# Kernel optimization log

Measured on AMD Instinct MI355X. Metric: run time of the kernel, lower is better.

## Reference

```python
import jax, jax.numpy as jnp
import numpy as np
from jax import lax

NUM_CLASSES = 80
STRIDES = (8, 16, 32, 64, 128)
PRE_NMS_THRESH = 0.05
PRE_NMS_TOPK = 1000
NMS_THRESH = 0.6
POST_NMS_TOPK = 100
NUM_CONVS = 4
CIN = 256
BATCH = 2
FEAT_SHAPES = ((100, 152), (50, 76), (25, 38), (13, 19), (7, 10))
CLASS_OFFSET = 10000.0  # coordinate offset for class-aware NMS


def conv3x3(x, w, b):
    # x: [B,C,H,W], w: [O,C,3,3] -> [B,O,H,W], stride 1, SAME padding
    y = lax.conv_general_dilated(x, w, (1, 1), 'SAME',
                                 dimension_numbers=('NCHW', 'OIHW', 'NCHW'))
    return y + b[None, :, None, None]


def tower(x, Ws, Bs):
    # sequence of (conv3x3 -> ReLU), norm='none'
    for i in range(Ws.shape[0]):
        x = jax.nn.relu(conv3x3(x, Ws[i], Bs[i]))
    return x


def compute_locations(h, w, stride):
    sx = jnp.arange(w, dtype=jnp.float32) * stride
    sy = jnp.arange(h, dtype=jnp.float32) * stride
    yy, xx = jnp.meshgrid(sy, sx, indexing='ij')
    return jnp.stack([xx.reshape(-1), yy.reshape(-1)], axis=1) + stride // 2  # [HW,2]


def nms_single(boxes, scores, classes):
    # boxes [N,4], scores [N] (>=0), classes [N] int. Greedy class-aware NMS.
    off = classes.astype(boxes.dtype) * CLASS_OFFSET
    b = boxes + off[:, None]
    area = (b[:, 2] - b[:, 0]) * (b[:, 3] - b[:, 1])

    def step(s, _):
        i = jnp.argmax(s)
        v = s[i]
        bi = b[i]
        lt = jnp.maximum(bi[:2], b[:, :2])
        rb = jnp.minimum(bi[2:], b[:, 2:])
        wh = jnp.maximum(rb - lt, 0.0)
        inter = wh[:, 0] * wh[:, 1]
        iou = inter / (area[i] + area - inter + 1e-9)
        s2 = jnp.where(iou > NMS_THRESH, -1.0, s).at[i].set(-1.0)
        return s2, (i, v)

    _, (idx, vals) = lax.scan(step, scores, None, length=POST_NMS_TOPK)
    valid = vals > 0.0
    out = jnp.concatenate(
        [boxes[idx], vals[:, None], classes[idx].astype(boxes.dtype)[:, None]], axis=1)
    return jnp.where(valid[:, None], out, 0.0)  # [POST_NMS_TOPK, 6]


def _forward(p3, p4, p5, p6, p7, cls_w, cls_b, box_w, box_b,
             logit_w, logit_b, pred_w, pred_b, ctr_w, ctr_b, scales):
    feats = (p3, p4, p5, p6, p7)
    boxes_all, scores_all, cls_all = [], [], []
    for l, x in enumerate(feats):
        # share_tower has 0 convs -> identity
        ct = tower(x, cls_w, cls_b)
        bt = tower(x, box_w, box_b)
        logits = conv3x3(ct, logit_w, logit_b)                   # [B,C,H,W]
        ctr = conv3x3(bt, ctr_w, ctr_b)                          # [B,1,H,W]
        reg = jax.nn.relu(conv3x3(bt, pred_w, pred_b) * scales[l])  # [B,4,H,W]
        B, _, H, W = logits.shape
        HW = H * W
        locs = compute_locations(H, W, STRIDES[l])               # [HW,2]
        cls_prob = jax.nn.sigmoid(logits).transpose(0, 2, 3, 1).reshape(B, HW, NUM_CLASSES)
        ctr_prob = jax.nn.sigmoid(ctr).reshape(B, HW, 1)
        s = cls_prob * ctr_prob                                  # thresh_with_ctr
        s = jnp.where(s > PRE_NMS_THRESH, s, 0.0)
        k = min(PRE_NMS_TOPK, HW * NUM_CLASSES)
        vals, idx = lax.top_k(s.reshape(B, HW * NUM_CLASSES), k)
        loc_idx = idx // NUM_CLASSES                             # [B,k]
        cls_idx = idx % NUM_CLASSES
        reg_f = reg.transpose(0, 2, 3, 1).reshape(B, HW, 4)
        reg_sel = jnp.take_along_axis(reg_f, loc_idx[..., None], axis=1)  # [B,k,4]
        loc_sel = locs[loc_idx]                                  # [B,k,2]
        boxes = jnp.stack([loc_sel[..., 0] - reg_sel[..., 0],
                           loc_sel[..., 1] - reg_sel[..., 1],
                           loc_sel[..., 0] + reg_sel[..., 2],
                           loc_sel[..., 1] + reg_sel[..., 3]], axis=-1)
        boxes_all.append(boxes)
        scores_all.append(jnp.sqrt(jnp.maximum(vals, 1e-12)))
        cls_all.append(cls_idx)
    boxes = jnp.concatenate(boxes_all, axis=1)    # [B,N,4]
    scores = jnp.concatenate(scores_all, axis=1)  # [B,N]
    classes = jnp.concatenate(cls_all, axis=1)    # [B,N]
    return jax.vmap(nms_single)(boxes, scores, classes)  # [B,POST_NMS_TOPK,6]


def setup_inputs() -> dict:
    key = jax.random.key(0)
    ks = jax.random.split(key, 12)
    std = 0.05  # larger than fcos init std=0.01 so decoded scores exceed the threshold
    inp = {}
    for i, (h, w) in enumerate(FEAT_SHAPES):
        inp[f'p{i + 3}'] = jax.random.normal(ks[i], (BATCH, CIN, h, w), dtype=jnp.float32)
    inp['cls_w'] = jax.random.normal(ks[5], (NUM_CONVS, CIN, CIN, 3, 3), dtype=jnp.float32) * std
    inp['cls_b'] = jnp.zeros((NUM_CONVS, CIN), dtype=jnp.float32)
    inp['box_w'] = jax.random.normal(ks[6], (NUM_CONVS, CIN, CIN, 3, 3), dtype=jnp.float32) * std
    inp['box_b'] = jnp.zeros((NUM_CONVS, CIN), dtype=jnp.float32)
    inp['logit_w'] = jax.random.normal(ks[7], (NUM_CLASSES, CIN, 3, 3), dtype=jnp.float32) * std
    inp['logit_b'] = jnp.zeros((NUM_CLASSES,), dtype=jnp.float32)
    inp['pred_w'] = jax.random.normal(ks[8], (4, CIN, 3, 3), dtype=jnp.float32) * std
    inp['pred_b'] = jnp.zeros((4,), dtype=jnp.float32)
    inp['ctr_w'] = jax.random.normal(ks[9], (1, CIN, 3, 3), dtype=jnp.float32) * std
    inp['ctr_b'] = jnp.zeros((1,), dtype=jnp.float32)
    inp['scales'] = jnp.ones((5,), dtype=jnp.float32)
    return inp


def reference(p3, p4, p5, p6, p7, cls_w, cls_b, box_w, box_b,
              logit_w, logit_b, pred_w, pred_b, ctr_w, ctr_b, scales):
    return _forward(p3, p4, p5, p6, p7, cls_w, cls_b, box_w, box_b,
                    logit_w, logit_b, pred_w, pred_b, ctr_w, ctr_b, scales)
```

## Files before the change

### kernel.cpp

```cpp
#include <hip/hip_runtime.h>
#include <stdint.h>
#include <math.h>

#define NCLS 80
#define TOTHW 20267
#define WLAYER 1179648ull

typedef _Float16 f16x8 __attribute__((ext_vector_type(8)));
typedef float f32x4 __attribute__((ext_vector_type(4)));
typedef short s16x8 __attribute__((ext_vector_type(8)));

static constexpr int cLW[5]    = {152,76,38,19,10};
static constexpr int cLH[5]    = {100,50,25,13,7};
static constexpr int cLHW[5]   = {15200,3800,950,247,70};
static constexpr int cLCUM[5]  = {0,15200,19000,19950,20197};
static constexpr int cLSTR[5]  = {8,16,32,64,128};
static constexpr int cCB[11]   = {0,123,246,278,310,319,328,331,334,335,336};
static constexpr int cPBASE[11]= {0,15744,31488,35584,39680,40832,41984,42368,42752,42880,43008};
static constexpr int cRCUM[11] = {0,100,200,250,300,325,350,363,376,383,390};
static constexpr int cCPX64[6] = {0,475,594,624,632,635};
#define NPXB64 635
#define SBE 11010048ull

__device__ __forceinline__ void split2(float y, unsigned short& h0, unsigned short& h1) {
  _Float16 b0 = (_Float16)y;
  float f0 = (float)b0;
  _Float16 b1 = (_Float16)((y - f0) * 2048.0f);
  h0 = __builtin_bit_cast(unsigned short, b0);
  h1 = __builtin_bit_cast(unsigned short, b1);
}

__device__ __forceinline__ void lds_hist_add(uint32_t* h, uint32_t bucket) {
  unsigned long long act = __ballot(1);
  int lane = (int)(threadIdx.x & 63u);
  int leader = __ffsll(act) - 1;
  uint32_t lb = (uint32_t)__shfl((int)bucket, leader, 64);
  unsigned long long same = __ballot(bucket == lb);
  if (same == act) {
    if (lane == leader) atomicAdd(&h[bucket], (uint32_t)__popcll(act));
  } else {
    atomicAdd(&h[bucket], 1u);
  }
}

__global__ void k_zero(unsigned short* X0, unsigned short* X1) {
  int px = blockIdx.x * 256 + threadIdx.x;
  if (px >= 43008) return;
  int pi = 0;
#pragma unroll
  for (int i = 1; i < 10; i++) if (px >= cPBASE[i]) pi = i;
  const int l = pi >> 1;
  const int p = px - cPBASE[pi];
  const int W = cLW[l], H = cLH[l], PWl = W + 2;
  const int pr = p / PWl, pc = p - pr * PWl;
  if (pr >= 1 && pr <= H && pc >= 1 && pc <= W) return;
  s16x8 z = {0,0,0,0,0,0,0,0};
  size_t base = (size_t)px * 256;
#pragma unroll
  for (int k = 0; k < 32; k++) {
    *reinterpret_cast<s16x8*>(X0 + base + k*8) = z;
    *reinterpret_cast<s16x8*>(X1 + base + k*8) = z;
  }
}

__global__ __launch_bounds__(256)
void k_prep(const float* __restrict__ p0, const float* __restrict__ p1,
            const float* __restrict__ p2, const float* __restrict__ p3,
            const float* __restrict__ p4,
            unsigned short* __restrict__ X0, unsigned short* __restrict__ X1) {
  int bx = blockIdx.x;
  int pi = 0;
#pragma unroll
  for (int i = 1; i < 10; i++) if (bx >= cRCUM[i]) pi = i;
  const int h = bx - cRCUM[pi];
  const int l = pi >> 1, bidx = pi & 1;
  const int W = cLW[l], HW = cLHW[l], PWl = W + 2;
  const int PB = cPBASE[pi];
  const float* src;
  if (l == 0) src = p0; else if (l == 1) src = p1; else if (l == 2) src = p2;
  else if (l == 3) src = p3; else src = p4;
  src += (size_t)bidx * 256 * HW;
  const int tid = threadIdx.x;
  __shared__ float tile[64][152];
  for (int c0 = 0; c0 < 256; c0 += 64) {
    {
      int c = tid >> 2, wq = tid & 3;
      for (int w = wq; w < W; w += 4)
        tile[c][w] = src[(size_t)(c0 + c) * HW + h * W + w];
    }
    __syncthreads();
    {
      int c8 = (tid & 7) * 8;
      for (int w = tid >> 3; w < W; w += 32) {
        size_t base = (size_t)(PB + (h + 1) * PWl + (w + 1)) * 256 + c0 + c8;
        unsigned short a0[8], a1[8];
#pragma unroll
        for (int j = 0; j < 8; j++) split2(tile[c8 + j][w], a0[j], a1[j]);
        *reinterpret_cast<s16x8*>(X0 + base) = *reinterpret_cast<s16x8*>(a0);
        *reinterpret_cast<s16x8*>(X1 + base) = *reinterpret_cast<s16x8*>(a1);
      }
    }
    __syncthreads();
  }
}

__global__ void k_packall(const float* __restrict__ box_w, const float* __restrict__ cls_w,
                          const float* __restrict__ logit_w, unsigned short* __restrict__ wp) {
  const int layer = blockIdx.y;
  const int oc = blockIdx.x, c = threadIdx.x;
  const float* w; int Cout = 256;
  const size_t WSTRIDE = (size_t)256 * 2304;
  if (layer < 4)      w = box_w + (size_t)layer * WSTRIDE;
  else if (layer < 8) w = cls_w + (size_t)(layer - 4) * WSTRIDE;
  else { w = logit_w; Cout = NCLS; }
  if (oc >= Cout) return;
  unsigned short* wpL = wp + (size_t)layer * WLAYER;
  const int ocf = oc >> 4, ln = oc & 15;
  const int kc = c >> 5, kg = (c >> 3) & 3, e = c & 7;
  const int lane = kg * 16 + ln;
#pragma unroll
  for (int r = 0; r < 9; r++) {
    float v = w[((size_t)oc * 256 + c) * 9 + r];
    unsigned short h0, h1;
    split2(v, h0, h1);
    wpL[((((size_t)(r * 2 + 0) * 16 + ocf) * 8 + kc) * 64 + lane) * 8 + e] = h0;
    wpL[((((size_t)(r * 2 + 1) * 16 + ocf) * 8 + kc) * 64 + lane) * 8 + e] = h1;
  }
}

__global__ void k_packhead(const float* __restrict__ ctw, const float* __restrict__ pdw,
                           float* __restrict__ wh) {
  const int r = blockIdx.x, c = threadIdx.x;
  float* d = &wh[((size_t)r * 256 + c) * 5];
  d[0] = ctw[c * 9 + r];
#pragma unroll
  for (int q = 0; q < 4; q++) d[1 + q] = pdw[(size_t)q * 2304 + c * 9 + r];
}

struct MfArgs {
  const unsigned short *X0, *X1;
  const unsigned short *Wp;
  const float* bias;
  unsigned short *Y0, *Y1;
  float* actf;
  float* scores;
  const float* ctrp;
  uint32_t* hist;
};

template<int EPI>
__global__ __launch_bounds__(256, 2)
void conv_mfma(MfArgs a) {
  __shared__ __align__(16) unsigned short lds[18432];
  const int tid = threadIdx.x;
  const int lane = tid & 63;
  const int wid = tid >> 6;

  const int nwg = (EPI == 2) ? 336 : 672;
  const int id = blockIdx.x;
  const int w = (id & 7) * (nwg >> 3) + (id >> 3);
  const int oc0 = (EPI == 2) ? 0 : (w & 1) * 128;
  int bx = (EPI == 2) ? w : (w >> 1);

  int pi = 0;
#pragma unroll
  for (int i = 1; i < 10; i++) if (bx >= cCB[i]) pi = i;
  const int l = pi >> 1, bidx = pi & 1;
  const int pxb = bx - cCB[pi];
  const int px0 = pxb * 128;
  const int PB = cPBASE[pi];
  const int W = cLW[l], H = cLH[l], HW = cLHW[l], PWl = W + 2;

  int row_[2], g_[2];
#pragma unroll
  for (int d = 0; d < 2; d++) {
    int idx2 = tid + d * 256;
    row_[d] = idx2 >> 2;
    g_[d] = idx2 & 3;
  }

  const int wr = wid >> 1, wc = wid & 1;
  const int kg = lane >> 4, ln15 = lane & 15;
  int fA[4];
#pragma unroll
  for (int mt = 0; mt < 4; mt++) fA[mt] = (wr * 64 + mt * 16 + ln15) * 72 + kg * 8;
  const int ocfb = (oc0 >> 4) + wc * 4;

  f32x4 acc0[4][4], acc1[4][4];
#pragma unroll
  for (int mt = 0; mt < 4; mt++)
#pragma unroll
    for (int nt = 0; nt < 4; nt++) {
      acc0[mt][nt] = (f32x4){0.f, 0.f, 0.f, 0.f};
      acc1[mt][nt] = (f32x4){0.f, 0.f, 0.f, 0.f};
    }

  s16x8 ra[4];
  auto loadA = [&](int step) {
    const int rr = step >> 3;
    const int c0 = (step & 7) << 5;
    const int dh = rr / 3 - 1, dw = rr - (rr / 3) * 3 - 1;
    const long long OFF = (long long)(PB + px0 + dh * PWl + dw);
#pragma unroll
    for (int s = 0; s < 2; s++) {
      const unsigned short* Xs = (s == 0) ? a.X0 : a.X1;
#pragma unroll
      for (int d = 0; d < 2; d++)
        ra[s * 2 + d] = *reinterpret_cast<const s16x8*>(Xs + (OFF + row_[d]) * 256 + c0 + g_[d] * 8);
    }
  };
  auto writeA = [&](int buf) {
#pragma unroll
    for (int s = 0; s < 2; s++)
#pragma unroll
      for (int d = 0; d < 2; d++) {
        const int o = buf * 9216 + row_[d] * 72 + (s * 4 + g_[d]) * 8;
        *reinterpret_cast<s16x8*>(&lds[o]) = ra[s * 2 + d];
      }
  };
  auto loadB = [&](int step, f16x8* bv) {
    const int rr = step >> 3, cc = step & 7;
#pragma unroll
    for (int nt = 0; nt < 4; nt++) {
      const size_t bo = ((size_t)((rr * 2) * 16 + ocfb + nt) * 8 + cc) * 512 + lane * 8;
      bv[nt * 2 + 0] = *reinterpret_cast<const f16x8*>(a.Wp + bo);
      bv[nt * 2 + 1] = *reinterpret_cast<const f16x8*>(a.Wp + bo + 65536);
    }
  };
  auto mfmaStep = [&](int buf, const f16x8* bv) {
    f16x8 av[4][2];
#pragma unroll
    for (int mt = 0; mt < 4; mt++) {
      av[mt][0] = *reinterpret_cast<const f16x8*>(&lds[buf * 9216 + fA[mt]]);
      av[mt][1] = *reinterpret_cast<const f16x8*>(&lds[buf * 9216 + fA[mt] + 32]);
    }
#pragma unroll
    for (int mt = 0; mt < 4; mt++)
#pragma unroll
      for (int nt = 0; nt < 4; nt++) {
        acc0[mt][nt] = __builtin_amdgcn_mfma_f32_16x16x32_f16(av[mt][0], bv[nt * 2 + 0], acc0[mt][nt], 0, 0, 0);
        acc1[mt][nt] = __builtin_amdgcn_mfma_f32_16x16x32_f16(av[mt][0], bv[nt * 2 + 1], acc1[mt][nt], 0, 0, 0);
        acc1[mt][nt] = __builtin_amdgcn_mfma_f32_16x16x32_f16(av[mt][1], bv[nt * 2 + 0], acc1[mt][nt], 0, 0, 0);
      }
  };

  f16x8 bv0[8], bv1[8];
  loadA(0); writeA(0);
  loadA(1);
  loadB(0, bv0);
  __syncthreads();

  for (int sp = 0; sp < 72; sp += 2) {
    if (sp + 1 < 72) { writeA(1); loadB(sp + 1, bv1); }
    if (sp + 2 < 72) loadA(sp + 2);
    mfmaStep(0, bv0);
    __syncthreads();
    if (sp + 2 < 72) { writeA(0); loadB(sp + 2, bv0); }
    if (sp + 3 < 72) loadA(sp + 3);
    mfmaStep(1, bv1);
    __syncthreads();
  }

  uint32_t* hh = nullptr;
  if (EPI == 2) {
    hh = reinterpret_cast<uint32_t*>(lds);
    for (int i = tid; i < 4096; i += 256) hh[i] = 0;
    __syncthreads();
  }
#pragma unroll
  for (int mt = 0; mt < 4; mt++) {
#pragma unroll
    for (int i = 0; i < 4; i++) {
      const int pxl = wr * 64 + mt * 16 + (lane >> 4) * 4 + i;
      const int p = px0 + pxl;
      const int pr = p / PWl, pc = p - pr * PWl;
      if (!(pr >= 1 && pr <= H && pc >= 1 && pc <= W)) continue;
      const int hw = (pr - 1) * W + (pc - 1);
#pragma unroll
      for (int nt = 0; nt < 4; nt++) {
        const int oc = oc0 + wc * 64 + nt * 16 + ln15;
        const float v = acc0[mt][nt][i] + acc1[mt][nt][i] * 4.8828125e-4f;
        if (EPI == 2) {
          if (oc < NCLS) {
            float y = v + a.bias[oc];
            float pcs = 1.0f / (1.0f + expf(-y));
            float s = pcs * a.ctrp[2 * cLCUM[l] + bidx * HW + hw];
            s = (s > 0.05f) ? s : 0.f;
            a.scores[(size_t)NCLS * (2 * cLCUM[l] + bidx * HW) + (size_t)oc * HW + hw] = s;
            lds_hist_add(hh, __float_as_uint(s) >> 20);
          }
        } else {
          float y = fmaxf(v + a.bias[oc], 0.f);
          if (EPI == 0) {
            size_t o = (size_t)(PB + p) * 256 + oc;
            unsigned short h0, h1;
            split2(y, h0, h1);
            a.Y0[o] = h0; a.Y1[o] = h1;
          } else {
            a.actf[(size_t)(PB + p) * 256 + oc] = y;
          }
        }
      }
    }
  }
  if (EPI == 2) {
    __syncthreads();
    uint32_t* gh = a.hist + (size_t)(l * 2 + bidx) * 4096;
    for (int i = tid; i < 4096; i += 256) { uint32_t v = hh[i]; if (v) atomicAdd(&gh[i], v); }
  }
}

__global__ __launch_bounds__(256)
void k_head2(const float* __restrict__ headact, const float* __restrict__ wh,
             const float* __restrict__ ctb, const float* __restrict__ pdb,
             const float* __restrict__ scl,
             float* __restrict__ ctrp, float* __restrict__ regb) {
  __shared__ float swh[11520];
  for (int i = threadIdx.x; i < 11520; i += 256) swh[i] = wh[i];
  int bx = blockIdx.x; int l = 0;
#pragma unroll
  for (int i = 1; i < 5; i++) if (bx >= cCPX64[i]) l = i;
  const int lblk = bx - cCPX64[l];
  const int H = cLH[l], W = cLW[l], HW = cLHW[l]; const int N = 2 * HW;
  const int lane = threadIdx.x & 63;
  const int wv = threadIdx.x >> 6;
  __syncthreads();
  const float bb0 = ctb[0], bb1 = pdb[0], bb2 = pdb[1], bb3 = pdb[2], bb4 = pdb[3];
  const float sc = scl[l];
  const int c4 = lane * 4;
  for (int t = 0; t < 16; ++t) {
    int px = lblk * 64 + wv * 16 + t;
    if (px >= N) break;
    int bb = px / HW; int hw = px - bb * HW; int hh = hw / W; int ww = hw - hh * W;
    const int PB = cPBASE[l * 2 + bb];
    float a0 = 0.f, a1 = 0.f, a2 = 0.f, a3 = 0.f, a4 = 0.f;
#pragma unroll
    for (int r = 0; r < 9; r++) {
      int dh = r / 3 - 1, dw = r % 3 - 1;
      int ih = hh + dh, iw = ww + dw;
      if (!(((unsigned)ih < (unsigned)H) && ((unsigned)iw < (unsigned)W))) continue;
      const float4 x = *reinterpret_cast<const float4*>(
          headact + (size_t)(PB + (ih + 1) * (W + 2) + (iw + 1)) * 256 + c4);
      const float* wr = &swh[(size_t)(r * 256 + c4) * 5];
      a0 = fmaf(x.x, wr[0],  a0); a1 = fmaf(x.x, wr[1],  a1); a2 = fmaf(x.x, wr[2],  a2);
      a3 = fmaf(x.x, wr[3],  a3); a4 = fmaf(x.x, wr[4],  a4);
      a0 = fmaf(x.y, wr[5],  a0); a1 = fmaf(x.y, wr[6],  a1); a2 = fmaf(x.y, wr[7],  a2);
      a3 = fmaf(x.y, wr[8],  a3); a4 = fmaf(x.y, wr[9],  a4);
      a0 = fmaf(x.z, wr[10], a0); a1 = fmaf(x.z, wr[11], a1); a2 = fmaf(x.z, wr[12], a2);
      a3 = fmaf(x.z, wr[13], a3); a4 = fmaf(x.z, wr[14], a4);
      a0 = fmaf(x.w, wr[15], a0); a1 = fmaf(x.w, wr[16], a1); a2 = fmaf(x.w, wr[17], a2);
      a3 = fmaf(x.w, wr[18], a3); a4 = fmaf(x.w, wr[19], a4);
    }
#pragma unroll
    for (int off = 32; off > 0; off >>= 1) {
      a0 += __shfl_xor(a0, off, 64); a1 += __shfl_xor(a1, off, 64); a2 += __shfl_xor(a2, off, 64);
      a3 += __shfl_xor(a3, off, 64); a4 += __shfl_xor(a4, off, 64);
    }
    if (lane == 0) {
      const int gi = 2 * cLCUM[l] + bb * HW + hw;
      ctrp[gi] = 1.0f / (1.0f + expf(-(a0 + bb0)));
      float* rg = regb + (size_t)gi * 4;
      rg[0] = fmaxf((a1 + bb1) * sc, 0.f);
      rg[1] = fmaxf((a2 + bb2) * sc, 0.f);
      rg[2] = fmaxf((a3 + bb3) * sc, 0.f);
      rg[3] = fmaxf((a4 + bb4) * sc, 0.f);
    }
  }
}

__global__ void k_init(uint32_t* __restrict__ hist, uint32_t* __restrict__ ctrA,
                       uint32_t* __restrict__ ctrB, uint32_t* __restrict__ survCnt) {
  int i = blockIdx.x * blockDim.x + threadIdx.x;
  if (i < 40960) hist[i] = 0;
  if (i < 10) { ctrA[i] = 0; ctrB[i] = 0; }
  if (i < 2) survCnt[i] = 0;
}

__global__ __launch_bounds__(256)
void k_select(const uint32_t* __restrict__ hist, int* __restrict__ meta) {
  const int sid = blockIdx.x;
  const uint32_t* gh = hist + (size_t)sid * 4096;
  __shared__ uint32_t ps[256];
  uint32_t sum = 0;
  for (int i = 0; i < 16; i++) sum += gh[threadIdx.x * 16 + i];
  ps[threadIdx.x] = sum;
  __syncthreads();
  if (threadIdx.x == 0) {
    uint32_t c = 0; int T = 0, m = 1000;
    for (int ch = 255; ch >= 0; --ch) {
      if (c + ps[ch] >= 1000u) {
        for (int t = ch * 16 + 15; t >= ch * 16; --t) {
          uint32_t hv = gh[t];
          if (c + hv >= 1000u) { T = t; m = (int)(1000u - c); break; }
          c += hv;
        }
        break;
      }
      c += ps[ch];
    }
    meta[sid * 4 + 0] = T;
    meta[sid * 4 + 1] = (int)c;
    meta[sid * 4 + 2] = m;
    meta[sid * 4 + 3] = (int)gh[T];
  }
}

__global__ __launch_bounds__(256)
void k_collect(const float* __restrict__ scores, const int* __restrict__ meta,
               unsigned long long* __restrict__ listA, unsigned long long* __restrict__ listB,
               uint32_t* __restrict__ ctrA, uint32_t* __restrict__ ctrB) {
  const int sid = blockIdx.y; const int l = sid >> 1, b = sid & 1;
  const int HW = cLHW[l]; const int size = NCLS * HW;
  const int base = blockIdx.x * 4096;
  if (base >= size) return;
  const size_t sbase = (size_t)NCLS * (2 * cLCUM[l] + b * HW);
  const float* sb = scores + sbase;
  unsigned long long* lB = listB + sbase;
  unsigned long long* lA = listA + (size_t)sid * 1024;
  const uint32_t T = (uint32_t)meta[sid * 4];
  const int lane = (int)(threadIdx.x & 63u);
  __shared__ uint32_t cA, cB, bA, bB;
  if (threadIdx.x == 0) { cA = 0; cB = 0; }
  __syncthreads();
  uint32_t wa = 0, wb = 0;
  for (int j = 0; j < 16; j++) {
    int i = base + threadIdx.x + j * 256;
    bool inb = (i < size);
    uint32_t bits = inb ? __float_as_uint(sb[i]) : 0u;
    uint32_t bkt = bits >> 20;
    unsigned long long mA = __ballot(inb && bkt > T);
    unsigned long long mB = __ballot(inb && bkt == T);
    if (lane == 0) { wa += (uint32_t)__popcll(mA); wb += (uint32_t)__popcll(mB); }
  }
  if (lane == 0) { if (wa) atomicAdd(&cA, wa); if (wb) atomicAdd(&cB, wb); }
  __syncthreads();
  if (threadIdx.x == 0) {
    bA = cA ? atomicAdd(&ctrA[sid], cA) : 0u;
    bB = cB ? atomicAdd(&ctrB[sid], cB) : 0u;
    cA = 0; cB = 0;
  }
  __syncthreads();
  for (int j = 0; j < 16; j++) {
    int i = base + threadIdx.x + j * 256;
    bool inb = (i < size);
    uint32_t bits = inb ? __float_as_uint(sb[i]) : 0u;
    uint32_t bkt = bits >> 20;
    bool pA = inb && bkt > T;
    bool pB = inb && bkt == T;
    unsigned long long key = 0;
    if (pA || pB) {
      int cls = i / HW; int hw = i - cls * HW;
      uint32_t idx = (uint32_t)(hw * NCLS + cls);
      key = ((unsigned long long)bits << 32) | (unsigned long long)(0xFFFFFFFFu - idx);
    }
    unsigned long long mA = __ballot(pA);
    unsigned long long mB = __ballot(pB);
    unsigned long long lt = (1ull << lane) - 1ull;
    if (mA) {
      int ld = __ffsll(mA) - 1;
      uint32_t wbs = 0;
      if (lane == ld) wbs = atomicAdd(&cA, (uint32_t)__popcll(mA));
      wbs = (uint32_t)__shfl((int)wbs, ld, 64);
      if (pA) {
        uint32_t pos = bA + wbs + (uint32_t)__popcll(mA & lt);
        if (pos < 1024u) lA[pos] = key;
      }
    }
    if (mB) {
      int ld = __ffsll(mB) - 1;
      uint32_t wbs = 0;
      if (lane == ld) wbs = atomicAdd(&cB, (uint32_t)__popcll(mB));
      wbs = (uint32_t)__shfl((int)wbs, ld, 64);
      if (pB) lB[bB + wbs + (uint32_t)__popcll(mB & lt)] = key;
    }
  }
}

__global__ __launch_bounds__(1024)
void k_refine(const int* __restrict__ meta, const unsigned long long* __restrict__ listB,
              unsigned long long* __restrict__ listA, uint32_t* __restrict__ ctrA) {
  const int sid = blockIdx.x; const int l = sid >> 1, b = sid & 1;
  const int HW = cLHW[l];
  const size_t sbase = (size_t)NCLS * (2 * cLCUM[l] + b * HW);
  const unsigned long long* lB = listB + sbase;
  const int nB = meta[sid * 4 + 3];
  int m = meta[sid * 4 + 2];
  __shared__ uint32_t h[256];
  __shared__ unsigned long long sPre;
  __shared__ int sM;
  __shared__ uint32_t sCnt;
  unsigned long long prefix = 0, mask = 0;
  for (int p = 7; p >= 0; --p) {
    for (int i = threadIdx.x; i < 256; i += 1024) h[i] = 0;
    __syncthreads();
    for (int i = threadIdx.x; i < nB; i += 1024) {
      unsigned long long k = lB[i];
      if ((k & mask) == prefix) {
        uint32_t bkt = (uint32_t)((k >> (p * 8)) & 255ull);
        lds_hist_add(h, bkt);
      }
    }
    __syncthreads();
    if (threadIdx.x == 0) {
      uint32_t c = 0; int sel = 0; int mnew = m;
      for (int t = 255; t >= 0; --t) {
        if (c + h[t] >= (uint32_t)m) { sel = t; mnew = m - (int)c; break; }
        c += h[t];
      }
      sPre = prefix | ((unsigned long long)sel << (p * 8));
      sM = mnew;
    }
    __syncthreads();
    prefix = sPre; m = sM;
    mask |= (0xFFull << (p * 8));
    __syncthreads();
  }
  if (threadIdx.x == 0) sCnt = ctrA[sid];
  __syncthreads();
  for (int i = threadIdx.x; i < nB; i += 1024) {
    unsigned long long k = lB[i];
    if (k >= prefix) {
      uint32_t pos = atomicAdd(&sCnt, 1u);
      if (pos < 1024u) listA[(size_t)sid * 1024 + pos] = k;
    }
  }
  __syncthreads();
  if (threadIdx.x == 0) ctrA[sid] = sCnt;
}

__global__ __launch_bounds__(256)
void k_sortdec(const unsigned long long* __restrict__ listA, const uint32_t* __restrict__ ctrA,
               const float* __restrict__ regb, float* __restrict__ cbox,
               float* __restrict__ cscr, float* __restrict__ ccls) {
  const int sid = blockIdx.x; const int l = sid >> 1, b = sid & 1;
  const int HW = cLHW[l], W = cLW[l];
  __shared__ unsigned long long key[1024];
  int n = (int)ctrA[sid]; if (n > 1024) n = 1024;
  for (int i = threadIdx.x; i < 1024; i += 256)
    key[i] = (i < n) ? listA[(size_t)sid * 1024 + i] : 0ull;
  __syncthreads();
  for (int len = 2; len <= 1024; len <<= 1) {
    for (int j = len >> 1; j > 0; j >>= 1) {
      for (int t = threadIdx.x; t < 512; t += 256) {
        int i = ((t & ~(j - 1)) << 1) | (t & (j - 1));
        int pp = i | j;
        unsigned long long a = key[i], bq = key[pp];
        bool desc = ((i & len) == 0);
        if ((a < bq) == desc) { key[i] = bq; key[pp] = a; }
      }
      __syncthreads();
    }
  }
  for (int r = threadIdx.x; r < 1000; r += 256) {
    unsigned long long k = key[r];
    uint32_t bits = (uint32_t)(k >> 32);
    uint32_t idx = 0xFFFFFFFFu - (uint32_t)(k & 0xFFFFFFFFull);
    float val = __uint_as_float(bits);
    float sc = sqrtf(fmaxf(val, 1e-12f));
    int cls = (int)(idx % NCLS); int loc = (int)(idx / NCLS);
    int hh = loc / W; int ww = loc - hh * W;
    float cx = (float)(ww * cLSTR[l] + (cLSTR[l] >> 1));
    float cy = (float)(hh * cLSTR[l] + (cLSTR[l] >> 1));
    const float* rg = regb + (size_t)(2 * cLCUM[l] + b * HW + loc) * 4;
    int slot = b * 5000 + l * 1000 + r;
    cbox[slot * 4 + 0] = cx - rg[0];
    cbox[slot * 4 + 1] = cy - rg[1];
    cbox[slot * 4 + 2] = cx + rg[2];
    cbox[slot * 4 + 3] = cy + rg[3];
    cscr[slot] = sc;
    ccls[slot] = (float)cls;
  }
}

#define NMSC 1536
__global__ __launch_bounds__(256)
void k_nmscls(const float* __restrict__ cbox, const float* __restrict__ cscr,
              const float* __restrict__ ccls,
              unsigned long long* __restrict__ surv, uint32_t* __restrict__ survCnt) {
  const int cls = blockIdx.x;
  const int b = blockIdx.y;
  __shared__ unsigned short mslot[5024];
  __shared__ float ms[5024];
  __shared__ float kx1[NMSC], ky1[NMSC], kx2[NMSC], ky2[NMSC], kar[NMSC];
  __shared__ uint32_t mcnt;
  __shared__ int sPick; __shared__ float sPickV;
  __shared__ float pb[5];
  __shared__ float wvv[4]; __shared__ int wvi[4];
  if (threadIdx.x == 0) mcnt = 0;
  __syncthreads();
  const float fc = (float)cls;
  for (int j = threadIdx.x; j < 5000; j += 256) {
    if (ccls[b * 5000 + j] == fc) {
      uint32_t p = atomicAdd(&mcnt, 1u);
      mslot[p] = (unsigned short)j;
      ms[p] = cscr[b * 5000 + j];
    }
  }
  __syncthreads();
  const int n = (int)mcnt;
  if (n == 0) return;
  const float off = fc * 10000.0f;
  const int nc = n < NMSC ? n : NMSC;
  for (int i = threadIdx.x; i < nc; i += 256) {
    const float4 bq = *reinterpret_cast<const float4*>(cbox + ((size_t)b * 5000 + mslot[i]) * 4);
    float x1 = bq.x + off, y1 = bq.y + off, x2 = bq.z + off, y2 = bq.w + off;
    kx1[i] = x1; ky1[i] = y1; kx2[i] = x2; ky2[i] = y2; kar[i] = (x2 - x1) * (y2 - y1);
  }
  __syncthreads();
  const int lane = threadIdx.x & 63, wv = threadIdx.x >> 6;
  for (int it = 0; it < 100; ++it) {
    float best = -1.f; int bi = 0x7FFF; int bidx = 0;
    for (int i = threadIdx.x; i < n; i += 256) {
      float v = ms[i];
      int sl = mslot[i];
      if (v > best || (v == best && sl < bi)) { best = v; bi = sl; bidx = i; }
    }
    for (int o = 32; o > 0; o >>= 1) {
      float ov = __shfl_down(best, o, 64);
      int oi = __shfl_down(bi, o, 64);
      int ox = __shfl_down(bidx, o, 64);
      if (ov > best || (ov == best && oi < bi)) { best = ov; bi = oi; bidx = ox; }
    }
    if (lane == 0) { wvv[wv] = best; wvi[wv] = (bidx << 13) | bi; }
    __syncthreads();
    if (threadIdx.x == 0) {
      float bb = wvv[0]; int pk = wvi[0];
      for (int q = 1; q < 4; q++) {
        float v = wvv[q]; int c = wvi[q];
        if (v > bb || (v == bb && (c & 8191) < (pk & 8191))) { bb = v; pk = c; }
      }
      sPickV = bb; sPick = pk;
      if (bb >= 0.f) {
        int slot = pk & 8191;
        uint32_t bits = __float_as_uint(bb);
        uint32_t gslot = (uint32_t)(b * 5000 + slot);
        unsigned long long key = ((unsigned long long)bits << 32) |
                                 (unsigned long long)(0xFFFFFFFFu - gslot);
        uint32_t pos = atomicAdd(&survCnt[b], 1u);
        surv[(size_t)b * 5000 + pos] = key;
        const float4 bx = *reinterpret_cast<const float4*>(cbox + (size_t)gslot * 4);
        pb[0] = bx.x + off; pb[1] = bx.y + off; pb[2] = bx.z + off; pb[3] = bx.w + off;
        pb[4] = (pb[2] - pb[0]) * (pb[3] - pb[1]);
      }
    }
    __syncthreads();
    if (sPickV < 0.f) break;
    const int pidx = sPick >> 13;
    const float bx1 = pb[0], by1 = pb[1], bx2 = pb[2], by2 = pb[3], ba = pb[4];
    for (int i = threadIdx.x; i < n; i += 256) {
      float v = ms[i];
      if (v < 0.f) continue;
      float x1, y1, x2, y2, ar;
      if (i < NMSC) {
        x1 = kx1[i]; y1 = ky1[i]; x2 = kx2[i]; y2 = ky2[i]; ar = kar[i];
      } else {
        const float4 bq = *reinterpret_cast<const float4*>(cbox + ((size_t)b * 5000 + mslot[i]) * 4);
        x1 = bq.x + off; y1 = bq.y + off; x2 = bq.z + off; y2 = bq.w + off;
        ar = (x2 - x1) * (y2 - y1);
      }
      float ix1 = fmaxf(bx1, x1), iy1 = fmaxf(by1, y1);
      float ix2 = fminf(bx2, x2), iy2 = fminf(by2, y2);
      float iw = fmaxf(ix2 - ix1, 0.f), ih = fmaxf(iy2 - iy1, 0.f);
      float inter = iw * ih;
      float iou = inter / ((ba + ar - inter) + 1e-9f);
      if (iou > 0.6f || i == pidx) ms[i] = -1.0f;
    }
    __syncthreads();
  }
}

__global__ __launch_bounds__(1024)
void k_nmsfinal(const unsigned long long* __restrict__ surv, const uint32_t* __restrict__ survCnt,
                const float* __restrict__ cbox, const float* __restrict__ ccls,
                float* __restrict__ out) {
  const int b = blockIdx.x;
  const int n = (int)survCnt[b];
  const unsigned long long* sv = surv + (size_t)b * 5000;
  const int m = n < 100 ? n : 100;
  __shared__ uint32_t h[256];
  __shared__ unsigned long long sPre; __shared__ int sM;
  __shared__ unsigned long long topk[128];
  __shared__ uint32_t tcnt;
  unsigned long long prefix = 0, mask = 0;
  int mm = m;
  if (m > 0) {
    for (int p = 7; p >= 0; --p) {
      for (int i = threadIdx.x; i < 256; i += 1024) h[i] = 0;
      __syncthreads();
      for (int i = threadIdx.x; i < n; i += 1024) {
        unsigned long long k = sv[i];
        if ((k & mask) == prefix) lds_hist_add(h, (uint32_t)((k >> (p * 8)) & 255ull));
      }
      __syncthreads();
      if (threadIdx.x == 0) {
        uint32_t c = 0; int sel = 0; int mnew = mm;
        for (int t = 255; t >= 0; --t) {
          if (c + h[t] >= (uint32_t)mm) { sel = t; mnew = mm - (int)c; break; }
          c += h[t];
        }
        sPre = prefix | ((unsigned long long)sel << (p * 8));
        sM = mnew;
      }
      __syncthreads();
      prefix = sPre; mm = sM;
      mask |= (0xFFull << (p * 8));
      __syncthreads();
    }
  }
  if (threadIdx.x == 0) tcnt = 0;
  for (int i = threadIdx.x; i < 128; i += 1024) topk[i] = 0;
  __syncthreads();
  if (m > 0) {
    for (int i = threadIdx.x; i < n; i += 1024) {
      unsigned long long k = sv[i];
      if (k >= prefix) {
        uint32_t p = atomicAdd(&tcnt, 1u);
        if (p < 128) topk[p] = k;
      }
    }
  }
  __syncthreads();
  for (int len = 2; len <= 128; len <<= 1) {
    for (int j = len >> 1; j > 0; j >>= 1) {
      for (int t = threadIdx.x; t < 64; t += 1024) {
        int i = ((t & ~(j - 1)) << 1) | (t & (j - 1));
        int pp = i | j;
        unsigned long long a = topk[i], bq = topk[pp];
        bool desc = ((i & len) == 0);
        if ((a < bq) == desc) { topk[i] = bq; topk[pp] = a; }
      }
      __syncthreads();
    }
  }
  if (threadIdx.x < 100) {
    int it = threadIdx.x;
    float* orow = out + ((size_t)b * 100 + it) * 6;
    if (it < m) {
      unsigned long long k = topk[it];
      uint32_t gslot = 0xFFFFFFFFu - (uint32_t)(k & 0xFFFFFFFFull);
      const float4 bx = *reinterpret_cast<const float4*>(cbox + (size_t)gslot * 4);
      orow[0] = bx.x; orow[1] = bx.y; orow[2] = bx.z; orow[3] = bx.w;
      orow[4] = __uint_as_float((uint32_t)(k >> 32));
      orow[5] = ccls[gslot];
    } else {
      orow[0] = 0.f; orow[1] = 0.f; orow[2] = 0.f;
      orow[3] = 0.f; orow[4] = 0.f; orow[5] = 0.f;
    }
  }
}

static inline size_t alignup(size_t x) { return (x + 255) & ~(size_t)255; }

extern "C" void kernel_launch(void* const* d_in, const int* in_sizes, int n_in,
                              void* d_out, int out_size, void* d_ws, size_t ws_size,
                              hipStream_t stream) {
  (void)in_sizes; (void)n_in; (void)out_size; (void)ws_size;
  const float* p0 = (const float*)d_in[0];
  const float* p1 = (const float*)d_in[1];
  const float* p2 = (const float*)d_in[2];
  const float* p3 = (const float*)d_in[3];
  const float* p4 = (const float*)d_in[4];
  const float* cls_w   = (const float*)d_in[5];
  const float* cls_b   = (const float*)d_in[6];
  const float* box_w   = (const float*)d_in[7];
  const float* box_b   = (const float*)d_in[8];
  const float* logit_w = (const float*)d_in[9];
  const float* logit_b = (const float*)d_in[10];
  const float* pred_w  = (const float*)d_in[11];
  const float* pred_b  = (const float*)d_in[12];
  const float* ctr_w   = (const float*)d_in[13];
  const float* ctr_b   = (const float*)d_in[14];
  const float* scales  = (const float*)d_in[15];

  char* base = (char*)d_ws;
  size_t off = 0;
  auto take = [&](size_t bytes) { void* p = base + off; off = alignup(off + bytes); return p; };
  float* regb = (float*)take((size_t)4 * 2 * TOTHW * 4);
  float* ctrp = (float*)take((size_t)2 * TOTHW * 4);
  uint32_t* hist = (uint32_t*)take((size_t)40960 * 4);
  int* meta = (int*)take((size_t)40 * 4);
  uint32_t* ctrA = (uint32_t*)take(256);
  uint32_t* ctrB = (uint32_t*)take(256);
  uint32_t* survCnt = (uint32_t*)take(256);
  unsigned long long* listA = (unsigned long long*)take((size_t)10 * 1024 * 8);
  unsigned long long* surv = (unsigned long long*)take((size_t)2 * 5000 * 8);
  float* cbox = (float*)take((size_t)2 * 5000 * 16);
  float* cscr = (float*)take((size_t)2 * 5000 * 4);
  float* ccls = (float*)take((size_t)2 * 5000 * 4);
  float* wh   = (float*)take((size_t)9 * 256 * 5 * 4);
  unsigned short* wpackF = (unsigned short*)take((size_t)9 * WLAYER * 2);
  unsigned short* P_0 = (unsigned short*)take(SBE * 2);
  unsigned short* P_1 = (unsigned short*)take(SBE * 2);
  unsigned short* R1_0 = (unsigned short*)take(SBE * 2);
  unsigned short* R1_1 = (unsigned short*)take(SBE * 2);
  unsigned short* R2_0 = (unsigned short*)take(SBE * 2);
  unsigned short* R2_1 = (unsigned short*)take(SBE * 2);
  (void)take(65536);
  float* scores = (float*)R1_0;
  unsigned long long* listB = (unsigned long long*)R2_0;
  float* headact = (float*)R2_0;

  hipLaunchKernelGGL(k_init, dim3(160), dim3(256), 0, stream, hist, ctrA, ctrB, survCnt);
  hipLaunchKernelGGL(k_packhead, dim3(9), dim3(256), 0, stream, ctr_w, pred_w, wh);
  hipLaunchKernelGGL(k_packall, dim3(256, 9), dim3(256), 0, stream, box_w, cls_w, logit_w, wpackF);
  hipLaunchKernelGGL(k_zero, dim3(168), dim3(256), 0, stream, P_0, P_1);
  hipLaunchKernelGGL(k_zero, dim3(168), dim3(256), 0, stream, R1_0, R1_1);
  hipLaunchKernelGGL(k_zero, dim3(168), dim3(256), 0, stream, R2_0, R2_1);
  hipLaunchKernelGGL(k_prep, dim3(390), dim3(256), 0, stream, p0, p1, p2, p3, p4, P_0, P_1);

  auto runConv = [&](int epi, int layer, const unsigned short* x0, const unsigned short* x1,
                     const float* bias, unsigned short* y0, unsigned short* y1,
                     float* af, float* sc) {
    MfArgs a;
    a.X0 = x0; a.X1 = x1; a.Wp = wpackF + (size_t)layer * WLAYER; a.bias = bias;
    a.Y0 = y0; a.Y1 = y1; a.actf = af; a.scores = sc; a.ctrp = ctrp;
    a.hist = hist;
    if (epi == 0)      hipLaunchKernelGGL(conv_mfma<0>, dim3(672), dim3(256), 0, stream, a);
    else if (epi == 1) hipLaunchKernelGGL(conv_mfma<1>, dim3(672), dim3(256), 0, stream, a);
    else               hipLaunchKernelGGL(conv_mfma<2>, dim3(336), dim3(256), 0, stream, a);
  };

  runConv(0, 0, P_0,  P_1,  box_b + 0,   R1_0, R1_1, nullptr, nullptr);
  runConv(0, 1, R1_0, R1_1, box_b + 256, R2_0, R2_1, nullptr, nullptr);
  runConv(0, 2, R2_0, R2_1, box_b + 512, R1_0, R1_1, nullptr, nullptr);
  runConv(1, 3, R1_0, R1_1, box_b + 768, nullptr, nullptr, headact, nullptr);
  hipLaunchKernelGGL(k_head2, dim3(NPXB64), dim3(256), 0, stream, headact, wh, ctr_b,
                     pred_b, scales, ctrp, regb);
  hipLaunchKernelGGL(k_zero, dim3(168), dim3(256), 0, stream, R2_0, R2_1);

  runConv(0, 4, P_0,  P_1,  cls_b + 0,   R1_0, R1_1, nullptr, nullptr);
  runConv(0, 5, R1_0, R1_1, cls_b + 256, R2_0, R2_1, nullptr, nullptr);
  runConv(0, 6, R2_0, R2_1, cls_b + 512, R1_0, R1_1, nullptr, nullptr);
  runConv(0, 7, R1_0, R1_1, cls_b + 768, R2_0, R2_1, nullptr, nullptr);
  runConv(2, 8, R2_0, R2_1, logit_b, nullptr, nullptr, nullptr, scores);

  hipLaunchKernelGGL(k_select,  dim3(10), dim3(256), 0, stream, hist, meta);
  hipLaunchKernelGGL(k_collect, dim3(297, 10), dim3(256), 0, stream, scores, meta, listA, listB, ctrA, ctrB);
  hipLaunchKernelGGL(k_refine,  dim3(10), dim3(1024), 0, stream, meta, listB, listA, ctrA);
  hipLaunchKernelGGL(k_sortdec, dim3(10), dim3(256), 0, stream, listA, ctrA, regb, cbox, cscr, ccls);
  hipLaunchKernelGGL(k_nmscls,  dim3(NCLS, 2), dim3(256), 0, stream, cbox, cscr, ccls, surv, survCnt);
  hipLaunchKernelGGL(k_nmsfinal, dim3(2), dim3(1024), 0, stream, surv, survCnt, cbox, ccls, (float*)d_out);
}
```

Baseline: 2.053 ms.

## Run box and cls tower convolutions together in one merged launch per layer

```diff
diff --git a/kernel.cpp b/kernel.cpp
--- a/kernel.cpp
+++ b/kernel.cpp
@@ -310,6 +310,159 @@
   }
 }
 
+struct Mf2Args {
+  const unsigned short *X0a, *X1a, *X0b, *X1b;
+  const unsigned short *Wpa, *Wpb;
+  const float *ba, *bb;
+  unsigned short *Y0a, *Y1a, *Y0b, *Y1b;
+  float* actf;
+};
+
+template<int LAST>
+__global__ __launch_bounds__(256, 2)
+void conv2_mfma(Mf2Args g) {
+  __shared__ __align__(16) unsigned short lds[18432];
+  const int tid = threadIdx.x;
+  const int lane = tid & 63;
+  const int wid = tid >> 6;
+
+  const int id = blockIdx.x;
+  const int w = (id & 7) * 168 + (id >> 3);
+  const int bx = w >> 2;
+  const int oc0 = (w & 1) * 128;
+  const int t = (w >> 1) & 1;
+  const unsigned short* X0 = t ? g.X0b : g.X0a;
+  const unsigned short* X1 = t ? g.X1b : g.X1a;
+  const unsigned short* Wp = t ? g.Wpb : g.Wpa;
+  const float* bias = t ? g.bb : g.ba;
+
+  int pi = 0;
+#pragma unroll
+  for (int i = 1; i < 10; i++) if (bx >= cCB[i]) pi = i;
+  const int l = pi >> 1;
+  const int pxb = bx - cCB[pi];
+  const int px0 = pxb * 128;
+  const int PB = cPBASE[pi];
+  const int W = cLW[l], H = cLH[l], PWl = W + 2;
+
+  int row_[2], g_[2];
+#pragma unroll
+  for (int d = 0; d < 2; d++) {
+    int idx2 = tid + d * 256;
+    row_[d] = idx2 >> 2;
+    g_[d] = idx2 & 3;
+  }
+
+  const int wr = wid >> 1, wc = wid & 1;
+  const int kg = lane >> 4, ln15 = lane & 15;
+  int fA[4];
+#pragma unroll
+  for (int mt = 0; mt < 4; mt++) fA[mt] = (wr * 64 + mt * 16 + ln15) * 72 + kg * 8;
+  const int ocfb = (oc0 >> 4) + wc * 4;
+
+  f32x4 acc0[4][4], acc1[4][4];
+#pragma unroll
+  for (int mt = 0; mt < 4; mt++)
+#pragma unroll
+    for (int nt = 0; nt < 4; nt++) {
+      acc0[mt][nt] = (f32x4){0.f, 0.f, 0.f, 0.f};
+      acc1[mt][nt] = (f32x4){0.f, 0.f, 0.f, 0.f};
+    }
+
+  s16x8 ra[4];
+  auto loadA = [&](int step) {
+    const int rr = step >> 3;
+    const int c0 = (step & 7) << 5;
+    const int dh = rr / 3 - 1, dw = rr - (rr / 3) * 3 - 1;
+    const long long OFF = (long long)(PB + px0 + dh * PWl + dw);
+#pragma unroll
+    for (int s = 0; s < 2; s++) {
+      const unsigned short* Xs = (s == 0) ? X0 : X1;
+#pragma unroll
+      for (int d = 0; d < 2; d++)
+        ra[s * 2 + d] = *reinterpret_cast<const s16x8*>(Xs + (OFF + row_[d]) * 256 + c0 + g_[d] * 8);
+    }
+  };
+  auto writeA = [&](int buf) {
+#pragma unroll
+    for (int s = 0; s < 2; s++)
+#pragma unroll
+      for (int d = 0; d < 2; d++) {
+        const int o = buf * 9216 + row_[d] * 72 + (s * 4 + g_[d]) * 8;
+        *reinterpret_cast<s16x8*>(&lds[o]) = ra[s * 2 + d];
+      }
+  };
+  auto loadB = [&](int step, f16x8* bv) {
+    const int rr = step >> 3, cc = step & 7;
+#pragma unroll
+    for (int nt = 0; nt < 4; nt++) {
+      const size_t bo = ((size_t)((rr * 2) * 16 + ocfb + nt) * 8 + cc) * 512 + lane * 8;
+      bv[nt * 2 + 0] = *reinterpret_cast<const f16x8*>(Wp + bo);
+      bv[nt * 2 + 1] = *reinterpret_cast<const f16x8*>(Wp + bo + 65536);
+    }
+  };
+  auto mfmaStep = [&](int buf, const f16x8* bv) {
+    f16x8 av[4][2];
+#pragma unroll
+    for (int mt = 0; mt < 4; mt++) {
+      av[mt][0] = *reinterpret_cast<const f16x8*>(&lds[buf * 9216 + fA[mt]]);
+      av[mt][1] = *reinterpret_cast<const f16x8*>(&lds[buf * 9216 + fA[mt] + 32]);
+    }
+#pragma unroll
+    for (int mt = 0; mt < 4; mt++)
+#pragma unroll
+      for (int nt = 0; nt < 4; nt++) {
+        acc0[mt][nt] = __builtin_amdgcn_mfma_f32_16x16x32_f16(av[mt][0], bv[nt * 2 + 0], acc0[mt][nt], 0, 0, 0);
+        acc1[mt][nt] = __builtin_amdgcn_mfma_f32_16x16x32_f16(av[mt][0], bv[nt * 2 + 1], acc1[mt][nt], 0, 0, 0);
+        acc1[mt][nt] = __builtin_amdgcn_mfma_f32_16x16x32_f16(av[mt][1], bv[nt * 2 + 0], acc1[mt][nt], 0, 0, 0);
+      }
+  };
+
+  f16x8 bv0[8], bv1[8];
+  loadA(0); writeA(0);
+  loadA(1);
+  loadB(0, bv0);
+  __syncthreads();
+
+  for (int sp = 0; sp < 72; sp += 2) {
+    if (sp + 1 < 72) { writeA(1); loadB(sp + 1, bv1); }
+    if (sp + 2 < 72) loadA(sp + 2);
+    mfmaStep(0, bv0);
+    __syncthreads();
+    if (sp + 2 < 72) { writeA(0); loadB(sp + 2, bv0); }
+    if (sp + 3 < 72) loadA(sp + 3);
+    mfmaStep(1, bv1);
+    __syncthreads();
+  }
+
+  unsigned short* Y0 = t ? g.Y0b : g.Y0a;
+  unsigned short* Y1 = t ? g.Y1b : g.Y1a;
+#pragma unroll
+  for (int mt = 0; mt < 4; mt++) {
+#pragma unroll
+    for (int i = 0; i < 4; i++) {
+      const int pxl = wr * 64 + mt * 16 + (lane >> 4) * 4 + i;
+      const int p = px0 + pxl;
+      const int pr = p / PWl, pc = p - pr * PWl;
+      if (!(pr >= 1 && pr <= H && pc >= 1 && pc <= W)) continue;
+#pragma unroll
+      for (int nt = 0; nt < 4; nt++) {
+        const int oc = oc0 + wc * 64 + nt * 16 + ln15;
+        const float v = acc0[mt][nt][i] + acc1[mt][nt][i] * 4.8828125e-4f;
+        float y = fmaxf(v + bias[oc], 0.f);
+        if (LAST && t == 0) {
+          g.actf[(size_t)(PB + p) * 256 + oc] = y;
+        } else {
+          size_t o = (size_t)(PB + p) * 256 + oc;
+          unsigned short h0, h1;
+          split2(y, h0, h1);
+          Y0[o] = h0; Y1[o] = h1;
+        }
+      }
+    }
+  }
+}
+
 __global__ __launch_bounds__(256)
 void k_head2(const float* __restrict__ headact, const float* __restrict__ wh,
              const float* __restrict__ ctb, const float* __restrict__ pdb,
@@ -754,7 +907,7 @@
 extern "C" void kernel_launch(void* const* d_in, const int* in_sizes, int n_in,
                               void* d_out, int out_size, void* d_ws, size_t ws_size,
                               hipStream_t stream) {
-  (void)in_sizes; (void)n_in; (void)out_size; (void)ws_size;
+  (void)in_sizes; (void)n_in; (void)out_size;
   const float* p0 = (const float*)d_in[0];
   const float* p1 = (const float*)d_in[1];
   const float* p2 = (const float*)d_in[2];
@@ -796,9 +949,13 @@
   unsigned short* R2_0 = (unsigned short*)take(SBE * 2);
   unsigned short* R2_1 = (unsigned short*)take(SBE * 2);
   (void)take(65536);
+  unsigned short* D_0 = (unsigned short*)take(SBE * 2);
+  unsigned short* D_1 = (unsigned short*)take(SBE * 2);
+  (void)take(65536);
+  const bool merged = (ws_size >= off);
+
   float* scores = (float*)R1_0;
   unsigned long long* listB = (unsigned long long*)R2_0;
-  float* headact = (float*)R2_0;
 
   hipLaunchKernelGGL(k_init, dim3(160), dim3(256), 0, stream, hist, ctrA, ctrB, survCnt);
   hipLaunchKernelGGL(k_packhead, dim3(9), dim3(256), 0, stream, ctr_w, pred_w, wh);
@@ -806,6 +963,7 @@
   hipLaunchKernelGGL(k_zero, dim3(168), dim3(256), 0, stream, P_0, P_1);
   hipLaunchKernelGGL(k_zero, dim3(168), dim3(256), 0, stream, R1_0, R1_1);
   hipLaunchKernelGGL(k_zero, dim3(168), dim3(256), 0, stream, R2_0, R2_1);
+  if (merged) hipLaunchKernelGGL(k_zero, dim3(168), dim3(256), 0, stream, D_0, D_1);
   hipLaunchKernelGGL(k_prep, dim3(390), dim3(256), 0, stream, p0, p1, p2, p3, p4, P_0, P_1);
 
   auto runConv = [&](int epi, int layer, const unsigned short* x0, const unsigned short* x1,
@@ -820,19 +978,43 @@
     else               hipLaunchKernelGGL(conv_mfma<2>, dim3(336), dim3(256), 0, stream, a);
   };
 
-  runConv(0, 0, P_0,  P_1,  box_b + 0,   R1_0, R1_1, nullptr, nullptr);
-  runConv(0, 1, R1_0, R1_1, box_b + 256, R2_0, R2_1, nullptr, nullptr);
-  runConv(0, 2, R2_0, R2_1, box_b + 512, R1_0, R1_1, nullptr, nullptr);
-  runConv(1, 3, R1_0, R1_1, box_b + 768, nullptr, nullptr, headact, nullptr);
-  hipLaunchKernelGGL(k_head2, dim3(NPXB64), dim3(256), 0, stream, headact, wh, ctr_b,
-                     pred_b, scales, ctrp, regb);
-  hipLaunchKernelGGL(k_zero, dim3(168), dim3(256), 0, stream, R2_0, R2_1);
-
-  runConv(0, 4, P_0,  P_1,  cls_b + 0,   R1_0, R1_1, nullptr, nullptr);
-  runConv(0, 5, R1_0, R1_1, cls_b + 256, R2_0, R2_1, nullptr, nullptr);
-  runConv(0, 6, R2_0, R2_1, cls_b + 512, R1_0, R1_1, nullptr, nullptr);
-  runConv(0, 7, R1_0, R1_1, cls_b + 768, R2_0, R2_1, nullptr, nullptr);
-  runConv(2, 8, R2_0, R2_1, logit_b, nullptr, nullptr, nullptr, scores);
+  if (merged) {
+    auto run2 = [&](int last, int layer,
+                    const unsigned short* xa0, const unsigned short* xa1,
+                    const unsigned short* xb0, const unsigned short* xb1,
+                    unsigned short* ya0, unsigned short* ya1,
+                    unsigned short* yb0, unsigned short* yb1, float* af) {
+      Mf2Args g;
+      g.X0a = xa0; g.X1a = xa1; g.X0b = xb0; g.X1b = xb1;
+      g.Wpa = wpackF + (size_t)layer * WLAYER;
+      g.Wpb = wpackF + (size_t)(4 + layer) * WLAYER;
+      g.ba = box_b + layer * 256; g.bb = cls_b + layer * 256;
+      g.Y0a = ya0; g.Y1a = ya1; g.Y0b = yb0; g.Y1b = yb1; g.actf = af;
+      if (last) hipLaunchKernelGGL(conv2_mfma<1>, dim3(1344), dim3(256), 0, stream, g);
+      else      hipLaunchKernelGGL(conv2_mfma<0>, dim3(1344), dim3(256), 0, stream, g);
+    };
+    run2(0, 0, P_0, P_1, P_0, P_1, R1_0, R1_1, R2_0, R2_1, nullptr);
+    run2(0, 1, R1_0, R1_1, R2_0, R2_1, D_0, D_1, P_0, P_1, nullptr);
+    run2(0, 2, D_0, D_1, P_0, P_1, R1_0, R1_1, R2_0, R2_1, nullptr);
+    run2(1, 3, R1_0, R1_1, R2_0, R2_1, nullptr, nullptr, P_0, P_1, (float*)D_0);
+    hipLaunchKernelGGL(k_head2, dim3(NPXB64), dim3(256), 0, stream, (const float*)D_0, wh,
+                       ctr_b, pred_b, scales, ctrp, regb);
+    runConv(2, 8, P_0, P_1, logit_b, nullptr, nullptr, nullptr, scores);
+  } else {
+    float* headact = (float*)R2_0;
+    runConv(0, 0, P_0,  P_1,  box_b + 0,   R1_0, R1_1, nullptr, nullptr);
+    runConv(0, 1, R1_0, R1_1, box_b + 256, R2_0, R2_1, nullptr, nullptr);
+    runConv(0, 2, R2_0, R2_1, box_b + 512, R1_0, R1_1, nullptr, nullptr);
+    runConv(1, 3, R1_0, R1_1, box_b + 768, nullptr, nullptr, headact, nullptr);
+    hipLaunchKernelGGL(k_head2, dim3(NPXB64), dim3(256), 0, stream, headact, wh, ctr_b,
+                       pred_b, scales, ctrp, regb);
+    hipLaunchKernelGGL(k_zero, dim3(168), dim3(256), 0, stream, R2_0, R2_1);
+    runConv(0, 4, P_0,  P_1,  cls_b + 0,   R1_0, R1_1, nullptr, nullptr);
+    runConv(0, 5, R1_0, R1_1, cls_b + 256, R2_0, R2_1, nullptr, nullptr);
+    runConv(0, 6, R2_0, R2_1, cls_b + 512, R1_0, R1_1, nullptr, nullptr);
+    runConv(0, 7, R1_0, R1_1, cls_b + 768, R2_0, R2_1, nullptr, nullptr);
+    runConv(2, 8, R2_0, R2_1, logit_b, nullptr, nullptr, nullptr, scores);
+  }
 
   hipLaunchKernelGGL(k_select,  dim3(10), dim3(256), 0, stream, hist, meta);
   hipLaunchKernelGGL(k_collect, dim3(297, 10), dim3(256), 0, stream, scores, meta, listA, listB, ctrA, ctrB);
```

Result: faster. 1.980 ms (-3.6%).
